# Performance work log

Hardware: AMD Instinct MI355X
Metric: run time of the kernel (lower is better)

The kernel has to match this reference:

```python
import jax, jax.numpy as jnp
import numpy as np
import math

B, S, D = 4, 2048, 1024
H = 1
HD = D // H  # head_dim == hidden_dim since num_heads=1 (required by source's phase_encoder Linear)
HALF = HD // 2
SYNC_LOSS_WEIGHT = 0.01


def setup_inputs() -> dict:
    key = jax.random.key(0)
    ks = jax.random.split(key, 11)
    wstd = 0.02
    inp = {
        "x": jax.random.normal(ks[0], (B, S, D), dtype=jnp.float32),
        "Wq": jax.random.normal(ks[1], (D, D), dtype=jnp.float32) * wstd,
        "bq": jnp.zeros((D,), jnp.float32),
        "Wk": jax.random.normal(ks[2], (D, D), dtype=jnp.float32) * wstd,
        "bk": jnp.zeros((D,), jnp.float32),
        "Wv": jax.random.normal(ks[3], (D, D), dtype=jnp.float32) * wstd,
        "bv": jnp.zeros((D,), jnp.float32),
        "Wp": jax.random.normal(ks[4], (D, D), dtype=jnp.float32) * wstd,
        "bp": jnp.zeros((D,), jnp.float32),
        "Wo": jax.random.normal(ks[5], (D, D), dtype=jnp.float32) * wstd,
        "bo": jnp.zeros((D,), jnp.float32),
        "bifurcation_param": jnp.asarray(1.0, jnp.float32),
        "phase_coupling": jnp.asarray(0.5, jnp.float32),
    }
    return inp


def _phase(t, Wp, bp):
    # t: [B,H,S,HD] -> instantaneous phase via angle(complex(first_half, second_half))
    pf = t @ Wp.T + bp
    re, im = pf[..., :HALF], pf[..., HALF:]
    return jnp.arctan2(im, re)  # [B,H,S,HALF]


def reference(x, Wq, bq, Wk, bk, Wv, bv, Wp, bp, Wo, bo, bifurcation_param, phase_coupling):
    b, s, d = x.shape
    Q = (x @ Wq.T + bq).reshape(b, s, H, HD).transpose(0, 2, 1, 3)  # [B,H,S,HD]
    K = (x @ Wk.T + bk).reshape(b, s, H, HD).transpose(0, 2, 1, 3)
    V = (x @ Wv.T + bv).reshape(b, s, H, HD).transpose(0, 2, 1, 3)

    scores = jnp.einsum("bhqd,bhkd->bhqk", Q, K) / math.sqrt(HD)

    pQ = _phase(Q, Wp, bp)
    pK = _phase(K, Wp, bp)
    # mean_d cos(pQ - pK) == (cos(pQ)@cos(pK)^T + sin(pQ)@sin(pK)^T) / HALF
    sync = (jnp.einsum("bhqd,bhkd->bhqk", jnp.cos(pQ), jnp.cos(pK))
            + jnp.einsum("bhqd,bhkd->bhqk", jnp.sin(pQ), jnp.sin(pK))) / HALF

    t = jnp.tanh(scores)
    bif = bifurcation_param * t * (1.0 - t)

    chaotic = scores + phase_coupling * sync + bif
    attn = jax.nn.softmax(chaotic, axis=-1)

    av = jnp.einsum("bhqk,bhkd->bhqd", attn, V)
    av = av.transpose(0, 2, 1, 3).reshape(b, s, d)
    out = av @ Wo.T + bo

    # torch.var default: unbiased (ddof=1), over last dim of sync
    sync_loss = SYNC_LOSS_WEIGHT * jnp.var(sync, axis=-1, ddof=1).mean()
    return out, sync_loss
```

## Files before the change

kernel.cpp:

```cpp
#include <hip/hip_runtime.h>
#include <hip/hip_bf16.h>
#include <math.h>

#define S_LEN 2048
#define D_MODEL 1024
#define N_BATCH 4
#define N_HALF 512

typedef unsigned short u16;
typedef __attribute__((ext_vector_type(8))) short bf16x8;
typedef __attribute__((ext_vector_type(4))) float f32x4;

__device__ inline u16 f2bf(float v) {
  __hip_bfloat16 h = __float2bfloat16(v);
  return *reinterpret_cast<u16*>(&h);
}
__device__ inline float bf2f(u16 u) {
  __hip_bfloat16 h = *reinterpret_cast<__hip_bfloat16*>(&u);
  return __bfloat162float(h);
}
__device__ inline void gl2lds16(const void* g, void* l) {
  __builtin_amdgcn_global_load_lds(
      (const __attribute__((address_space(1))) unsigned int*)g,
      (__attribute__((address_space(3))) unsigned int*)l, 16, 0, 0);
}
__device__ inline float fast_tanh(float x) {
  float e = __expf(2.0f * x);
  return 1.0f - 2.0f / (e + 1.0f);
}
__device__ inline int xcd_swz(int hw, int n) {
  return (hw & 7) * (n >> 3) + (hw >> 3);
}


#define N0_X   (2097152LL)
#define NW_W   (262144LL)
__global__ __launch_bounds__(256)
void cast_bf4_multi(const float* __restrict__ sx, u16* __restrict__ dx,
                    const float* __restrict__ s1, u16* __restrict__ d1,
                    const float* __restrict__ s2, u16* __restrict__ d2,
                    const float* __restrict__ s3, u16* __restrict__ d3,
                    const float* __restrict__ s4, u16* __restrict__ d4h,
                    u16* __restrict__ d4l) {
  long long i = (long long)blockIdx.x * 256 + threadIdx.x;
  if (i < N0_X) {
    float4 v = ((const float4*)sx)[i];
    ushort4 o;
    o.x = f2bf(v.x); o.y = f2bf(v.y); o.z = f2bf(v.z); o.w = f2bf(v.w);
    ((ushort4*)dx)[i] = o;
    return;
  }
  long long k = i - N0_X;
  int w = (int)(k >> 18);
  long long off = k & (NW_W - 1);
  if (w < 3) {
    const float* s = (w == 0) ? s1 : (w == 1) ? s2 : s3;
    u16* d        = (w == 0) ? d1 : (w == 1) ? d2 : d3;
    float4 v = ((const float4*)s)[off];
    ushort4 o;
    o.x = f2bf(v.x); o.y = f2bf(v.y); o.z = f2bf(v.z); o.w = f2bf(v.w);
    ((ushort4*)d)[off] = o;
  } else {
    float4 v = ((const float4*)s4)[off];
    ushort4 oh, ol;
    float f;
    oh.x = f2bf(v.x); f = v.x - bf2f(oh.x); ol.x = f2bf(f);
    oh.y = f2bf(v.y); f = v.y - bf2f(oh.y); ol.y = f2bf(f);
    oh.z = f2bf(v.z); f = v.z - bf2f(oh.z); ol.z = f2bf(f);
    oh.w = f2bf(v.w); f = v.w - bf2f(oh.w); ol.w = f2bf(f);
    ((ushort4*)d4h)[off] = oh;
    ((ushort4*)d4l)[off] = ol;
  }
}
__global__ __launch_bounds__(256)
void cast_split(const float* __restrict__ src, u16* __restrict__ hi,
                u16* __restrict__ lo, long long n4) {
  long long i = (long long)blockIdx.x * 256 + threadIdx.x;
  if (i >= n4) return;
  float4 v = ((const float4*)src)[i];
  ushort4 oh, ol;
  float f;
  oh.x = f2bf(v.x); f = v.x - bf2f(oh.x); ol.x = f2bf(f);
  oh.y = f2bf(v.y); f = v.y - bf2f(oh.y); ol.y = f2bf(f);
  oh.z = f2bf(v.z); f = v.z - bf2f(oh.z); ol.z = f2bf(f);
  oh.w = f2bf(v.w); f = v.w - bf2f(oh.w); ol.w = f2bf(f);
  ((ushort4*)hi)[i] = oh;
  ((ushort4*)lo)[i] = ol;
}
__global__ __launch_bounds__(256)
void transpose_split(const float* __restrict__ src, u16* __restrict__ hi,
                     u16* __restrict__ lo) {
  __shared__ float t[32][33];
  const int bx = blockIdx.x * 32;
  const int by = blockIdx.y * 32;
  const int c = threadIdx.x & 31;
  const int r0 = (threadIdx.x >> 5) * 4;
#pragma unroll
  for (int r = 0; r < 4; r++)
    t[r0 + r][c] = src[(long long)(by + r0 + r) * D_MODEL + bx + c];
  __syncthreads();
#pragma unroll
  for (int r = 0; r < 4; r++) {
    float v = t[c][r0 + r];
    long long idx = (long long)(bx + r0 + r) * D_MODEL + by + c;
    u16 h = f2bf(v);
    hi[idx] = h;
    lo[idx] = f2bf(v - bf2f(h));
  }
}
__global__ __launch_bounds__(256)
void w2_bias(const float* __restrict__ Wo, const float* __restrict__ bv,
             float* __restrict__ w2b) {
  const int d = blockIdx.x;
  const int tid = threadIdx.x;
  float acc = 0.f;
  for (int j = tid; j < D_MODEL; j += 256)
    acc += Wo[(long long)d * D_MODEL + j] * bv[j];
#pragma unroll
  for (int m = 1; m < 64; m <<= 1) acc += __shfl_xor(acc, m);
  __shared__ float red[4];
  if ((tid & 63) == 0) red[tid >> 6] = acc;
  __syncthreads();
  if (tid == 0) w2b[d] = red[0] + red[1] + red[2] + red[3];
}

__global__ __launch_bounds__(256, 2)
void qk_out3(const u16* __restrict__ X, const u16* __restrict__ Wq,
             const u16* __restrict__ Wk,
             const float* __restrict__ bq, const float* __restrict__ bk,
             u16* __restrict__ Qo, u16* __restrict__ Ko,
             const u16* __restrict__ Ah3, const u16* __restrict__ Al3,
             const u16* __restrict__ Bh3, const u16* __restrict__ Bl3,
             float* __restrict__ W2f) {
  __shared__ __align__(16) u16 smem[4 * 128 * 64];
  const int id   = blockIdx.x;
  const int tid  = threadIdx.x;
  const int wave = tid >> 6;
  const int lane = tid & 63;
  const int quad = lane >> 4;
  const int tc   = lane & 15;
  const int wm = (wave & 1) * 64;
  const int wn = (wave >> 1) * 64;
  const int srow8 = lane >> 3;
  const int scol  = ((lane & 7) ^ srow8) * 8;
  const int srowb = wave * 32;
  const int wb = srowb * 64;
  const long long r8 = 8LL * D_MODEL;
  const int swzA = tc & 7;

  if (id < 64) {
    u16* Ash = smem;
    u16* Asl = smem + 8192;
    u16* Bsh = smem + 16384;
    u16* Bsl = smem + 24576;
    const int bm = (id >> 3) * 128;
    const int bn = (id & 7) * 128;

    f32x4 acc[4][4];
#pragma unroll
    for (int i = 0; i < 4; i++)
#pragma unroll
      for (int j = 0; j < 4; j++) acc[i][j] = (f32x4){0.f, 0.f, 0.f, 0.f};

    long long aoff = (long long)(bm + srowb + srow8) * D_MODEL + scol;
    long long boff = (long long)(bn + srowb + srow8) * D_MODEL + scol;
    const u16 *gah = Ah3 + aoff, *gal = Al3 + aoff;
    const u16 *gbh = Bh3 + boff, *gbl = Bl3 + boff;

    for (int k0 = 0; k0 < D_MODEL; k0 += 64) {
#pragma unroll
      for (int c = 0; c < 4; c++) {
        gl2lds16(gah + c * r8, Ash + wb + c * 512);
        gl2lds16(gal + c * r8, Asl + wb + c * 512);
        gl2lds16(gbh + c * r8, Bsh + wb + c * 512);
        gl2lds16(gbl + c * r8, Bsl + wb + c * 512);
      }
      gah += 64; gal += 64; gbh += 64; gbl += 64;
      __syncthreads();
      bf16x8 ah[4][2], al[4][2], bh[4][2], bl[4][2];
#pragma unroll
      for (int i = 0; i < 4; i++) {
        const int ra = (wm + i * 16 + tc) * 64;
        const int rb = (wn + i * 16 + tc) * 64;
#pragma unroll
        for (int ks = 0; ks < 2; ks++) {
          const int co = ((ks * 4 + quad) ^ swzA) * 8;
          ah[i][ks] = *(const bf16x8*)(Ash + ra + co);
          al[i][ks] = *(const bf16x8*)(Asl + ra + co);
          bh[i][ks] = *(const bf16x8*)(Bsh + rb + co);
          bl[i][ks] = *(const bf16x8*)(Bsl + rb + co);
        }
      }
#pragma unroll
      for (int i = 0; i < 4; i++)
#pragma unroll
        for (int j = 0; j < 4; j++) {
#pragma unroll
          for (int ks = 0; ks < 2; ks++) {
            acc[i][j] = __builtin_amdgcn_mfma_f32_16x16x32_bf16(ah[i][ks], bh[j][ks], acc[i][j], 0, 0, 0);
            acc[i][j] = __builtin_amdgcn_mfma_f32_16x16x32_bf16(ah[i][ks], bl[j][ks], acc[i][j], 0, 0, 0);
            acc[i][j] = __builtin_amdgcn_mfma_f32_16x16x32_bf16(al[i][ks], bh[j][ks], acc[i][j], 0, 0, 0);
          }
        }
      __syncthreads();
    }
#pragma unroll
    for (int i = 0; i < 4; i++) {
      const int row0 = bm + wm + i * 16 + quad * 4;
#pragma unroll
      for (int j = 0; j < 4; j++) {
        const int col = bn + wn + j * 16 + tc;
#pragma unroll
        for (int r = 0; r < 4; r++)
          W2f[(long long)(row0 + r) * D_MODEL + col] = acc[i][j][r];
      }
    }
  } else {
    u16* Xs = smem;
    u16* Qs = smem + 8192;
    u16* Ks = smem + 16384;
    const int qid = xcd_swz(id - 64, 512);
    const int bn = (qid & 7) * 128;
    const int bm = (qid >> 3) * 128;

    f32x4 acc1[4][4], acc2[4][4];
#pragma unroll
    for (int i = 0; i < 4; i++)
#pragma unroll
      for (int j = 0; j < 4; j++) {
        acc1[i][j] = (f32x4){0.f, 0.f, 0.f, 0.f};
        acc2[i][j] = (f32x4){0.f, 0.f, 0.f, 0.f};
      }

    const u16* gx = X  + (long long)(bm + srowb + srow8) * D_MODEL + scol;
    const u16* gq = Wq + (long long)(bn + srowb + srow8) * D_MODEL + scol;
    const u16* gk = Wk + (long long)(bn + srowb + srow8) * D_MODEL + scol;

    for (int k0 = 0; k0 < D_MODEL; k0 += 64) {
#pragma unroll
      for (int c = 0; c < 4; c++) {
        gl2lds16(gx + c * r8, Xs + wb + c * 512);
        gl2lds16(gq + c * r8, Qs + wb + c * 512);
        gl2lds16(gk + c * r8, Ks + wb + c * 512);
      }
      gx += 64; gq += 64; gk += 64;
      __syncthreads();
      bf16x8 af[4][2], bq4[4][2], bk4[4][2];
#pragma unroll
      for (int i = 0; i < 4; i++) {
        const int ra = (wm + i * 16 + tc) * 64;
        const int rb = (wn + i * 16 + tc) * 64;
#pragma unroll
        for (int ks = 0; ks < 2; ks++) {
          const int co = ((ks * 4 + quad) ^ swzA) * 8;
          af[i][ks]  = *(const bf16x8*)(Xs + ra + co);
          bq4[i][ks] = *(const bf16x8*)(Qs + rb + co);
          bk4[i][ks] = *(const bf16x8*)(Ks + rb + co);
        }
      }
#pragma unroll
      for (int i = 0; i < 4; i++)
#pragma unroll
        for (int j = 0; j < 4; j++) {
          acc1[i][j] = __builtin_amdgcn_mfma_f32_16x16x32_bf16(af[i][0], bq4[j][0], acc1[i][j], 0, 0, 0);
          acc2[i][j] = __builtin_amdgcn_mfma_f32_16x16x32_bf16(af[i][0], bk4[j][0], acc2[i][j], 0, 0, 0);
          acc1[i][j] = __builtin_amdgcn_mfma_f32_16x16x32_bf16(af[i][1], bq4[j][1], acc1[i][j], 0, 0, 0);
          acc2[i][j] = __builtin_amdgcn_mfma_f32_16x16x32_bf16(af[i][1], bk4[j][1], acc2[i][j], 0, 0, 0);
        }
      __syncthreads();
    }

#pragma unroll
    for (int i = 0; i < 4; i++) {
      const int row0 = bm + wm + i * 16 + quad * 4;
#pragma unroll
      for (int j = 0; j < 4; j++) {
        const int col = bn + wn + j * 16 + tc;
#pragma unroll
        for (int r = 0; r < 4; r++) {
          long long idx = (long long)(row0 + r) * D_MODEL + col;
          Qo[idx] = f2bf(acc1[i][j][r] + bq[col]);
          Ko[idx] = f2bf(acc2[i][j][r] + bk[col]);
        }
      }
    }
  }
}

__global__ __launch_bounds__(256, 2)
void pf_fused(const u16* __restrict__ Qb, const u16* __restrict__ Wp,
              const float* __restrict__ bp,
              u16* __restrict__ pfQ, u16* __restrict__ pfK,
              long long TDo) {
  __shared__ u16 lds_all[3 * 128 * 64];
  u16* Qs = lds_all;
  u16* Ks = lds_all + 128 * 64;
  u16* Ws = lds_all + 2 * 128 * 64;
  const int tid  = threadIdx.x;
  const int wave = tid >> 6;
  const int lane = tid & 63;
  const int quad = lane >> 4;
  const int tc   = lane & 15;
  const int oid = xcd_swz(blockIdx.x, 512);
  const int bm = (oid >> 3) * 128;
  const int bn = (oid & 7) * 64;
  const int wm = (wave & 1) * 64;
  const int grp = wave >> 1;

  f32x4 acc1[4][4], acc2[4][4];
#pragma unroll
  for (int i = 0; i < 4; i++)
#pragma unroll
    for (int j = 0; j < 4; j++) {
      acc1[i][j] = (f32x4){0.f, 0.f, 0.f, 0.f};
      acc2[i][j] = (f32x4){0.f, 0.f, 0.f, 0.f};
    }

  const int srow8 = lane >> 3;
  const int scol  = ((lane & 7) ^ srow8) * 8;
  const int srowb = wave * 32;
  const u16* gq = Qb + (long long)(bm + srowb + srow8) * D_MODEL + scol;
  const u16* gk = gq + TDo;
  const u16* gw = Wp + (long long)(bn + srowb + srow8 + ((wave & 2) ? 448 : 0)) * D_MODEL + scol;
  const int wb = srowb * 64;
  const long long r8 = 8LL * D_MODEL;
  const int swzA = tc & 7;

  for (int k0 = 0; k0 < D_MODEL; k0 += 64) {
#pragma unroll
    for (int c = 0; c < 4; c++) {
      gl2lds16(gq + c * r8, Qs + wb + c * 512);
      gl2lds16(gk + c * r8, Ks + wb + c * 512);
      gl2lds16(gw + c * r8, Ws + wb + c * 512);
    }
    gq += 64; gk += 64; gw += 64;
    __syncthreads();
    bf16x8 aq[4][2], ak[4][2], bw[4][2];
    const int wn = grp * 64;
#pragma unroll
    for (int i = 0; i < 4; i++) {
      const int ra = (wm + i * 16 + tc) * 64;
      const int rb = (wn + i * 16 + tc) * 64;
#pragma unroll
      for (int ks = 0; ks < 2; ks++) {
        const int co = ((ks * 4 + quad) ^ swzA) * 8;
        aq[i][ks] = *(const bf16x8*)(Qs + ra + co);
        ak[i][ks] = *(const bf16x8*)(Ks + ra + co);
        bw[i][ks] = *(const bf16x8*)(Ws + rb + co);
      }
    }
#pragma unroll
    for (int i = 0; i < 4; i++)
#pragma unroll
      for (int j = 0; j < 4; j++) {
        acc1[i][j] = __builtin_amdgcn_mfma_f32_16x16x32_bf16(aq[i][0], bw[j][0], acc1[i][j], 0, 0, 0);
        acc2[i][j] = __builtin_amdgcn_mfma_f32_16x16x32_bf16(ak[i][0], bw[j][0], acc2[i][j], 0, 0, 0);
        acc1[i][j] = __builtin_amdgcn_mfma_f32_16x16x32_bf16(aq[i][1], bw[j][1], acc1[i][j], 0, 0, 0);
        acc2[i][j] = __builtin_amdgcn_mfma_f32_16x16x32_bf16(ak[i][1], bw[j][1], acc2[i][j], 0, 0, 0);
      }
    __syncthreads();
  }

  float* ex = (float*)lds_all;
  const long long colbase = (long long)bn + (long long)grp * 512;
#pragma unroll
  for (int o = 0; o < 2; o++) {
    u16* Ou = o ? pfK : pfQ;
#pragma unroll
    for (int half = 0; half < 2; half++) {
      int cnt = 0;
#pragma unroll
      for (int i = 2 * half; i < 2 * half + 2; i++)
#pragma unroll
        for (int j = 0; j < 4; j++) {
          f32x4 v = o ? acc2[i][j] : acc1[i][j];
          float b = bp[colbase + j * 16 + tc];
          v[0] += b; v[1] += b; v[2] += b; v[3] += b;
          *(f32x4*)(ex + wave * 2048 + cnt * 256 + lane * 4) = v;
          cnt++;
        }
      __syncthreads();
      cnt = 0;
#pragma unroll
      for (int i = 2 * half; i < 2 * half + 2; i++)
#pragma unroll
        for (int j = 0; j < 4; j++) {
          f32x4 own = *(const f32x4*)(ex + wave * 2048 + cnt * 256 + lane * 4);
          f32x4 oth = *(const f32x4*)(ex + (wave ^ 2) * 2048 + cnt * 256 + lane * 4);
          const int row0 = bm + wm + i * 16 + quad * 4;
          const long long col = colbase + j * 16 + tc;
#pragma unroll
          for (int r = 0; r < 4; r++) {
            float a = own[r], p = oth[r];
            float n2 = a * a + p * p;
            float outv = (grp == 0) ? 1.f : 0.f;
            if (n2 > 0.f) outv = a * (1.0f / sqrtf(n2));
            Ou[(long long)(row0 + r) * D_MODEL + col] = f2bf(outv);
          }
          cnt++;
        }
      __syncthreads();
    }
  }
}

__global__ __launch_bounds__(256, 2)
void chaotic_vwt(const u16* __restrict__ Q, const u16* __restrict__ Kt,
                 const u16* __restrict__ Uq, const u16* __restrict__ Uk,
                 float* __restrict__ Cc,
                 float* __restrict__ ssum, float* __restrict__ ssq,
                 const float* __restrict__ bifp, const float* __restrict__ pcp,
                 const u16* __restrict__ W2h, const u16* __restrict__ W2l,
                 const u16* __restrict__ X, const float* __restrict__ w2b,
                 u16* __restrict__ Ch, u16* __restrict__ Cl,
                 long long sB, long long sC,
                 int interleave, int nchao) {
  __shared__ __align__(16) u16 smem[4 * 128 * 64];
  const int id = xcd_swz(blockIdx.x, (int)gridDim.x);
  int cid = -1, vid = -1;
  if (interleave) {
    if ((id % 3) == 2) vid = id / 3;
    else cid = (id / 3) * 2 + (id % 3);
  } else {
    if (id < nchao) cid = id; else vid = id - nchao;
  }

  const int tid  = threadIdx.x;
  const int wave = tid >> 6;
  const int lane = tid & 63;
  const int quad = lane >> 4;
  const int tc   = lane & 15;
  const int wm = (wave & 1) * 64;
  const int wn = (wave >> 1) * 64;
  const int srow8 = lane >> 3;
  const int scol  = ((lane & 7) ^ srow8) * 8;
  const int srowb = wave * 32;
  const int wb = srowb * 64;
  const long long r8 = 8LL * D_MODEL;
  const int swzA = tc & 7;

  if (cid >= 0) {
    u16* Qs = smem;
    u16* Ks = smem + 8192;
    u16* Us = smem + 16384;
    u16* Ws = smem + 24576;
    const int bn = (cid & 15) * 128;
    const int bm = ((cid >> 4) & 15) * 128;
    const long long z = cid >> 8;
    const long long sQ = (long long)S_LEN * D_MODEL;

    f32x4 acc1[4][4], acc2[4][4];
#pragma unroll
    for (int i = 0; i < 4; i++)
#pragma unroll
      for (int j = 0; j < 4; j++) {
        acc1[i][j] = (f32x4){0.f, 0.f, 0.f, 0.f};
        acc2[i][j] = (f32x4){0.f, 0.f, 0.f, 0.f};
      }

    const u16* gq = Q  + z * sQ + (long long)(bm + srowb + srow8) * D_MODEL + scol;
    const u16* gk = Kt + z * sQ + (long long)(bn + srowb + srow8) * D_MODEL + scol;
    const u16* gu = Uq + z * sQ + (long long)(bm + srowb + srow8) * D_MODEL + scol;
    const u16* gw = Uk + z * sQ + (long long)(bn + srowb + srow8) * D_MODEL + scol;

    for (int k0 = 0; k0 < D_MODEL; k0 += 64) {
#pragma unroll
      for (int c = 0; c < 4; c++) {
        gl2lds16(gq + c * r8, Qs + wb + c * 512);
        gl2lds16(gk + c * r8, Ks + wb + c * 512);
        gl2lds16(gu + c * r8, Us + wb + c * 512);
        gl2lds16(gw + c * r8, Ws + wb + c * 512);
      }
      gq += 64; gk += 64; gu += 64; gw += 64;
      __syncthreads();
      {
        bf16x8 af[4][2], bg[4][2];
#pragma unroll
        for (int i = 0; i < 4; i++) {
          const int ra = (wm + i * 16 + tc) * 64;
          const int rb = (wn + i * 16 + tc) * 64;
#pragma unroll
          for (int ks = 0; ks < 2; ks++) {
            const int co = ((ks * 4 + quad) ^ swzA) * 8;
            af[i][ks] = *(const bf16x8*)(Qs + ra + co);
            bg[i][ks] = *(const bf16x8*)(Ks + rb + co);
          }
        }
#pragma unroll
        for (int i = 0; i < 4; i++)
#pragma unroll
          for (int j = 0; j < 4; j++) {
            acc1[i][j] = __builtin_amdgcn_mfma_f32_16x16x32_bf16(af[i][0], bg[j][0], acc1[i][j], 0, 0, 0);
            acc1[i][j] = __builtin_amdgcn_mfma_f32_16x16x32_bf16(af[i][1], bg[j][1], acc1[i][j], 0, 0, 0);
          }
      }
      {
        bf16x8 cf[4][2], dg[4][2];
#pragma unroll
        for (int i = 0; i < 4; i++) {
          const int ra = (wm + i * 16 + tc) * 64;
          const int rb = (wn + i * 16 + tc) * 64;
#pragma unroll
          for (int ks = 0; ks < 2; ks++) {
            const int co = ((ks * 4 + quad) ^ swzA) * 8;
            cf[i][ks] = *(const bf16x8*)(Us + ra + co);
            dg[i][ks] = *(const bf16x8*)(Ws + rb + co);
          }
        }
#pragma unroll
        for (int i = 0; i < 4; i++)
#pragma unroll
          for (int j = 0; j < 4; j++) {
            acc2[i][j] = __builtin_amdgcn_mfma_f32_16x16x32_bf16(cf[i][0], dg[j][0], acc2[i][j], 0, 0, 0);
            acc2[i][j] = __builtin_amdgcn_mfma_f32_16x16x32_bf16(cf[i][1], dg[j][1], acc2[i][j], 0, 0, 0);
          }
      }
      __syncthreads();
    }

    const float bif = *bifp;
    const float pc  = *pcp;
    float rsum[4][4], rsq[4][4];
#pragma unroll
    for (int i = 0; i < 4; i++)
#pragma unroll
      for (int r = 0; r < 4; r++) { rsum[i][r] = 0.f; rsq[i][r] = 0.f; }

    float* C = Cc + z * (long long)S_LEN * S_LEN;
#pragma unroll
    for (int i = 0; i < 4; i++) {
      const int row0 = bm + wm + i * 16 + quad * 4;
#pragma unroll
      for (int j = 0; j < 4; j++) {
        const int col = bn + wn + j * 16 + tc;
#pragma unroll
        for (int r = 0; r < 4; r++) {
          float sc = acc1[i][j][r] * 0.03125f;
          float sy = acc2[i][j][r] * (1.0f / 512.0f);
          float t  = fast_tanh(sc);
          C[(long long)(row0 + r) * S_LEN + col] = sc + pc * sy + bif * t * (1.0f - t);
          rsum[i][r] += sy;
          rsq[i][r]  += sy * sy;
        }
      }
    }
#pragma unroll
    for (int m = 1; m < 16; m <<= 1) {
#pragma unroll
      for (int i = 0; i < 4; i++)
#pragma unroll
        for (int r = 0; r < 4; r++) {
          rsum[i][r] += __shfl_xor(rsum[i][r], m);
          rsq[i][r]  += __shfl_xor(rsq[i][r], m);
        }
    }
    if (tc == 0) {
#pragma unroll
      for (int i = 0; i < 4; i++)
#pragma unroll
        for (int r = 0; r < 4; r++) {
          long long rr = z * S_LEN + bm + wm + i * 16 + quad * 4 + r;
          atomicAdd(&ssum[rr], rsum[i][r]);
          atomicAdd(&ssq[rr],  rsq[i][r]);
        }
    }
  } else {
    u16* Ah = smem;
    u16* Al = smem + 8192;
    u16* Bs = smem + 16384;
    const int bn = (vid & 15) * 128;
    const int bm = ((vid >> 4) & 7) * 128;
    const long long z = vid >> 7;

    f32x4 acc[4][4];
#pragma unroll
    for (int i = 0; i < 4; i++)
#pragma unroll
      for (int j = 0; j < 4; j++) acc[i][j] = (f32x4){0.f, 0.f, 0.f, 0.f};

    const long long aoff = (long long)(bm + srowb + srow8) * D_MODEL + scol;
    const u16* gah = W2h + aoff;
    const u16* gal = W2l + aoff;
    const u16* gb  = X + z * sB + (long long)(bn + srowb + srow8) * D_MODEL + scol;

    for (int k0 = 0; k0 < D_MODEL; k0 += 64) {
#pragma unroll
      for (int c = 0; c < 4; c++) {
        gl2lds16(gah + c * r8, Ah + wb + c * 512);
        gl2lds16(gal + c * r8, Al + wb + c * 512);
        gl2lds16(gb  + c * r8, Bs + wb + c * 512);
      }
      gah += 64; gal += 64; gb += 64;
      __syncthreads();
      bf16x8 ah4[4][2], al4[4][2], bx[4][2];
#pragma unroll
      for (int i = 0; i < 4; i++) {
        const int ra = (wm + i * 16 + tc) * 64;
        const int rb = (wn + i * 16 + tc) * 64;
#pragma unroll
        for (int ks = 0; ks < 2; ks++) {
          const int co = ((ks * 4 + quad) ^ swzA) * 8;
          ah4[i][ks] = *(const bf16x8*)(Ah + ra + co);
          al4[i][ks] = *(const bf16x8*)(Al + ra + co);
          bx[i][ks]  = *(const bf16x8*)(Bs + rb + co);
        }
      }
#pragma unroll
      for (int i = 0; i < 4; i++)
#pragma unroll
        for (int j = 0; j < 4; j++) {
          acc[i][j] = __builtin_amdgcn_mfma_f32_16x16x32_bf16(ah4[i][0], bx[j][0], acc[i][j], 0, 0, 0);
          acc[i][j] = __builtin_amdgcn_mfma_f32_16x16x32_bf16(al4[i][0], bx[j][0], acc[i][j], 0, 0, 0);
          acc[i][j] = __builtin_amdgcn_mfma_f32_16x16x32_bf16(ah4[i][1], bx[j][1], acc[i][j], 0, 0, 0);
          acc[i][j] = __builtin_amdgcn_mfma_f32_16x16x32_bf16(al4[i][1], bx[j][1], acc[i][j], 0, 0, 0);
        }
      __syncthreads();
    }

    u16* Chz = Ch + z * sC;
    u16* Clz = Cl + z * sC;
#pragma unroll
    for (int i = 0; i < 4; i++) {
      const int row0 = bm + wm + i * 16 + quad * 4;
#pragma unroll
      for (int j = 0; j < 4; j++) {
        const int col = bn + wn + j * 16 + tc;
#pragma unroll
        for (int r = 0; r < 4; r++) {
          float v = acc[i][j][r] + w2b[row0 + r];
          long long idx = (long long)(row0 + r) * S_LEN + col;
          u16 h = f2bf(v);
          Chz[idx] = h;
          Clz[idx] = f2bf(v - bf2f(h));
        }
      }
    }
  }
}

__global__ __launch_bounds__(256)
void gemm_bsplit(const u16* __restrict__ A,
                 const u16* __restrict__ Bh, const u16* __restrict__ Bl,
                 const float* __restrict__ bias, float* __restrict__ C,
                 int N, int K, long long sA, long long sB, long long sC) {
  __shared__ u16 As[128 * 64];
  __shared__ u16 Bsh[128 * 64];
  __shared__ u16 Bsl[128 * 64];
  const int tid  = threadIdx.x;
  const int wave = tid >> 6;
  const int lane = tid & 63;
  const int quad = lane >> 4;
  const int tc   = lane & 15;
  const int oid = xcd_swz(blockIdx.x, (int)gridDim.x);
  const int bn = (oid & 7) * 128;
  const int bm = ((oid >> 3) & 15) * 128;
  const long long z = oid >> 7;
  const int wm = (wave & 1) * 64;
  const int wn = (wave >> 1) * 64;

  f32x4 acc[4][4];
#pragma unroll
  for (int i = 0; i < 4; i++)
#pragma unroll
    for (int j = 0; j < 4; j++) acc[i][j] = (f32x4){0.f, 0.f, 0.f, 0.f};

  const int srow8 = lane >> 3;
  const int scol  = ((lane & 7) ^ srow8) * 8;
  const int srowb = wave * 32;
  const long long boff = (long long)(bn + srowb + srow8) * K + scol;
  const u16* ga  = A + z * sA + (long long)(bm + srowb + srow8) * K + scol;
  const u16* gbh = Bh + z * sB + boff;
  const u16* gbl = Bl + z * sB + boff;
  const int wb = srowb * 64;
  const long long r8K = 8LL * K;
  const int swzA = tc & 7;

  for (int k0 = 0; k0 < K; k0 += 64) {
#pragma unroll
    for (int c = 0; c < 4; c++) {
      gl2lds16(ga  + c * r8K, As  + wb + c * 512);
      gl2lds16(gbh + c * r8K, Bsh + wb + c * 512);
      gl2lds16(gbl + c * r8K, Bsl + wb + c * 512);
    }
    ga += 64; gbh += 64; gbl += 64;
    __syncthreads();
    bf16x8 af[4][2], bh[4][2], bl[4][2];
#pragma unroll
    for (int i = 0; i < 4; i++) {
      const int ra = (wm + i * 16 + tc) * 64;
      const int rb = (wn + i * 16 + tc) * 64;
#pragma unroll
      for (int ks = 0; ks < 2; ks++) {
        const int co = ((ks * 4 + quad) ^ swzA) * 8;
        af[i][ks] = *(const bf16x8*)(As  + ra + co);
        bh[i][ks] = *(const bf16x8*)(Bsh + rb + co);
        bl[i][ks] = *(const bf16x8*)(Bsl + rb + co);
      }
    }
#pragma unroll
    for (int i = 0; i < 4; i++)
#pragma unroll
      for (int j = 0; j < 4; j++) {
        acc[i][j] = __builtin_amdgcn_mfma_f32_16x16x32_bf16(af[i][0], bh[j][0], acc[i][j], 0, 0, 0);
        acc[i][j] = __builtin_amdgcn_mfma_f32_16x16x32_bf16(af[i][0], bl[j][0], acc[i][j], 0, 0, 0);
        acc[i][j] = __builtin_amdgcn_mfma_f32_16x16x32_bf16(af[i][1], bh[j][1], acc[i][j], 0, 0, 0);
        acc[i][j] = __builtin_amdgcn_mfma_f32_16x16x32_bf16(af[i][1], bl[j][1], acc[i][j], 0, 0, 0);
      }
    __syncthreads();
  }

  float* Cz = C + z * sC;
#pragma unroll
  for (int i = 0; i < 4; i++) {
    const int row0 = bm + wm + i * 16 + quad * 4;
#pragma unroll
    for (int j = 0; j < 4; j++) {
      const int col = bn + wn + j * 16 + tc;
#pragma unroll
      for (int r = 0; r < 4; r++)
        Cz[(long long)(row0 + r) * N + col] = acc[i][j][r] + bias[col];
    }
  }
}

__global__ __launch_bounds__(256)
void softmax_bf(const float* __restrict__ Cc, u16* __restrict__ P) {
  const long long row = (long long)blockIdx.y * S_LEN + blockIdx.x;
  const int tid = threadIdx.x;
  const float* p = Cc + row * S_LEN + tid * 8;
  u16* q = P + row * S_LEN + tid * 8;
  float4 a = *(const float4*)p;
  float4 b = *(const float4*)(p + 4);
  float v[8] = {a.x, a.y, a.z, a.w, b.x, b.y, b.z, b.w};
  float m = v[0];
#pragma unroll
  for (int i = 1; i < 8; i++) m = fmaxf(m, v[i]);
#pragma unroll
  for (int mask = 1; mask < 64; mask <<= 1) m = fmaxf(m, __shfl_xor(m, mask));
  __shared__ float red[8];
  if ((tid & 63) == 0) red[tid >> 6] = m;
  __syncthreads();
  m = fmaxf(fmaxf(red[0], red[1]), fmaxf(red[2], red[3]));
  float s = 0.f;
#pragma unroll
  for (int i = 0; i < 8; i++) { v[i] = __expf(v[i] - m); s += v[i]; }
#pragma unroll
  for (int mask = 1; mask < 64; mask <<= 1) s += __shfl_xor(s, mask);
  __syncthreads();
  if ((tid & 63) == 0) red[4 + (tid >> 6)] = s;
  __syncthreads();
  s = red[4] + red[5] + red[6] + red[7];
  float inv = 1.0f / s;
  ushort4 o0, o1;
  o0.x = f2bf(v[0] * inv); o0.y = f2bf(v[1] * inv);
  o0.z = f2bf(v[2] * inv); o0.w = f2bf(v[3] * inv);
  o1.x = f2bf(v[4] * inv); o1.y = f2bf(v[5] * inv);
  o1.z = f2bf(v[6] * inv); o1.w = f2bf(v[7] * inv);
  *(ushort4*)q = o0;
  *(ushort4*)(q + 4) = o1;
}

__global__ __launch_bounds__(1024)
void syncloss_kernel(const float* __restrict__ ssum, const float* __restrict__ ssq,
                     float* __restrict__ out) {
  const int tid = threadIdx.x;
  float acc = 0.f;
  for (int r = tid; r < N_BATCH * S_LEN; r += 1024) {
    float su = ssum[r], sq = ssq[r];
    acc += (sq - su * su * (1.0f / 2048.0f)) * (1.0f / 2047.0f);
  }
#pragma unroll
  for (int mask = 1; mask < 64; mask <<= 1) acc += __shfl_xor(acc, mask);
  __shared__ float red[16];
  if ((tid & 63) == 0) red[tid >> 6] = acc;
  __syncthreads();
  if (tid == 0) {
    float t = 0.f;
#pragma unroll
    for (int k = 0; k < 16; k++) t += red[k];
    out[0] = 0.01f * (t / (float)(N_BATCH * S_LEN));
  }
}

extern "C" void kernel_launch(void* const* d_in, const int* in_sizes, int n_in,
                              void* d_out, int out_size, void* d_ws, size_t ws_size,
                              hipStream_t stream) {
  const float* x    = (const float*)d_in[0];
  const float* Wq   = (const float*)d_in[1];
  const float* bq   = (const float*)d_in[2];
  const float* Wk   = (const float*)d_in[3];
  const float* bk   = (const float*)d_in[4];
  const float* Wv   = (const float*)d_in[5];
  const float* bv   = (const float*)d_in[6];
  const float* Wp   = (const float*)d_in[7];
  const float* bp   = (const float*)d_in[8];
  const float* Wo   = (const float*)d_in[9];
  const float* bo   = (const float*)d_in[10];
  const float* bifp = (const float*)d_in[11];
  const float* pcp  = (const float*)d_in[12];
  float* out = (float*)d_out;

  const long long NROW = (long long)N_BATCH * S_LEN;
  const long long TD   = NROW * D_MODEL;
  const long long WSZ  = (long long)D_MODEL * D_MODEL;

  u16* xbf   = (u16*)d_ws;
  u16* wqb   = xbf + TD;
  u16* wkb   = wqb + WSZ;
  u16* wpb   = wkb + WSZ;
  u16* woh   = wpb + WSZ;
  u16* wol   = woh + WSZ;
  u16* wvth  = wol + WSZ;
  u16* wvtl  = wvth + WSZ;
  u16* w2h   = wvtl + WSZ;
  u16* w2l   = w2h + WSZ;
  float* W2f = (float*)(w2l + WSZ);
  float* w2b = W2f + WSZ;
  u16* Qbf   = (u16*)(w2b + D_MODEL);
  u16* Kbf   = Qbf + TD;
  u16* pfQ   = Kbf + TD;
  u16* pfK   = pfQ + TD;
  float* Cc  = (float*)(pfK + TD);
  float* ssum = Cc + (long long)N_BATCH * S_LEN * S_LEN;
  float* ssq  = ssum + NROW;
  u16* attn = Qbf;
  u16* vwh  = pfQ;
  u16* vwl  = pfK;
  u16* vwh2 = (u16*)(ssq + NROW);
  u16* vwl2 = vwh2 + TD;
  const size_t need = (size_t)((char*)(vwl2 + TD) - (char*)d_ws);
  const bool fused = (ws_size >= need);

  dim3 blk(256);
  const long long sQ = (long long)S_LEN * D_MODEL;
  const long long sS = (long long)S_LEN * S_LEN;

  cast_bf4_multi<<<12288, blk, 0, stream>>>(x, xbf, Wq, wqb, Wk, wkb, Wp, wpb,
                                            Wo, woh, wol);
  transpose_split<<<dim3(32, 32), blk, 0, stream>>>(Wv, wvth, wvtl);
  qk_out3<<<576, blk, 0, stream>>>(xbf, wqb, wkb, bq, bk, Qbf, Kbf,
                                   woh, wol, wvth, wvtl, W2f);
  cast_split<<<(int)(WSZ / 4 / 256), blk, 0, stream>>>(W2f, w2h, w2l, WSZ / 4);
  w2_bias<<<D_MODEL, blk, 0, stream>>>(Wo, bv, w2b);

  pf_fused<<<512, blk, 0, stream>>>(Qbf, wpb, bp, pfQ, pfK, TD);
  hipMemsetAsync(ssum, 0, (size_t)(2 * NROW) * sizeof(float), stream);

  if (fused) {
    chaotic_vwt<<<1536, blk, 0, stream>>>(
        Qbf, Kbf, pfQ, pfK, Cc, ssum, ssq, bifp, pcp,
        w2h, w2l, xbf, w2b, vwh2, vwl2, sQ, sQ, 1, 1024);
  } else {
    chaotic_vwt<<<1024, blk, 0, stream>>>(
        Qbf, Kbf, pfQ, pfK, Cc, ssum, ssq, bifp, pcp,
        w2h, w2l, xbf, w2b, vwh, vwl, sQ, sQ, 0, 1024);
    chaotic_vwt<<<512, blk, 0, stream>>>(
        Qbf, Kbf, pfQ, pfK, Cc, ssum, ssq, bifp, pcp,
        w2h, w2l, xbf, w2b, vwh, vwl, sQ, sQ, 0, 0);
  }

  softmax_bf<<<dim3(S_LEN, N_BATCH), blk, 0, stream>>>(Cc, attn);
  gemm_bsplit<<<512, blk, 0, stream>>>(
      attn, fused ? vwh2 : vwh, fused ? vwl2 : vwl, bo, out,
      D_MODEL, S_LEN, sS, sQ, sQ);
  syncloss_kernel<<<1, 1024, 0, stream>>>(ssum, ssq, out + TD);
}
```

Measured before the change: 444.8 us.

## Merge prep kernels, fuse hi/lo split into GEMM epilogue, remap tiles for L2 locality

Folds the cast, Wv transpose-split and Wo·bv bias kernels into one prep launch, and writes the W2 product directly as bf16 hi/lo from the qk_out3 epilogue, which removes the cast_split kernel and the fp32 W2f round trip. It also remaps block-to-tile indices in several GEMMs into grouped 4x4 or 2x4 supertiles within each chunk to improve L2 reuse of A and B tiles. The cost is more branching in a single large prep kernel, and the transpose path there now shares a block with a shared-memory barrier.

```diff
diff --git a/kernel.cpp b/kernel.cpp
--- a/kernel.cpp
+++ b/kernel.cpp
@@ -36,92 +36,84 @@
 #define N0_X   (2097152LL)
 #define NW_W   (262144LL)
 __global__ __launch_bounds__(256)
-void cast_bf4_multi(const float* __restrict__ sx, u16* __restrict__ dx,
-                    const float* __restrict__ s1, u16* __restrict__ d1,
-                    const float* __restrict__ s2, u16* __restrict__ d2,
-                    const float* __restrict__ s3, u16* __restrict__ d3,
-                    const float* __restrict__ s4, u16* __restrict__ d4h,
-                    u16* __restrict__ d4l) {
-  long long i = (long long)blockIdx.x * 256 + threadIdx.x;
-  if (i < N0_X) {
-    float4 v = ((const float4*)sx)[i];
-    ushort4 o;
-    o.x = f2bf(v.x); o.y = f2bf(v.y); o.z = f2bf(v.z); o.w = f2bf(v.w);
-    ((ushort4*)dx)[i] = o;
+void prep_multi(const float* __restrict__ sx, u16* __restrict__ dx,
+                const float* __restrict__ s1, u16* __restrict__ d1,
+                const float* __restrict__ s2, u16* __restrict__ d2,
+                const float* __restrict__ s3, u16* __restrict__ d3,
+                const float* __restrict__ s4, u16* __restrict__ d4h,
+                u16* __restrict__ d4l,
+                const float* __restrict__ Wv, u16* __restrict__ wvth,
+                u16* __restrict__ wvtl,
+                const float* __restrict__ Wo, const float* __restrict__ bv,
+                float* __restrict__ w2b) {
+  __shared__ float tsh[32][33];
+  const int bid = blockIdx.x;
+  const int tid = threadIdx.x;
+  if (bid < 12288) {
+    long long i = (long long)bid * 256 + tid;
+    if (i < N0_X) {
+      float4 v = ((const float4*)sx)[i];
+      ushort4 o;
+      o.x = f2bf(v.x); o.y = f2bf(v.y); o.z = f2bf(v.z); o.w = f2bf(v.w);
+      ((ushort4*)dx)[i] = o;
+      return;
+    }
+    long long k = i - N0_X;
+    int w = (int)(k >> 18);
+    long long off = k & (NW_W - 1);
+    if (w < 3) {
+      const float* s = (w == 0) ? s1 : (w == 1) ? s2 : s3;
+      u16* d        = (w == 0) ? d1 : (w == 1) ? d2 : d3;
+      float4 v = ((const float4*)s)[off];
+      ushort4 o;
+      o.x = f2bf(v.x); o.y = f2bf(v.y); o.z = f2bf(v.z); o.w = f2bf(v.w);
+      ((ushort4*)d)[off] = o;
+    } else {
+      float4 v = ((const float4*)s4)[off];
+      ushort4 oh, ol;
+      float f;
+      oh.x = f2bf(v.x); f = v.x - bf2f(oh.x); ol.x = f2bf(f);
+      oh.y = f2bf(v.y); f = v.y - bf2f(oh.y); ol.y = f2bf(f);
+      oh.z = f2bf(v.z); f = v.z - bf2f(oh.z); ol.z = f2bf(f);
+      oh.w = f2bf(v.w); f = v.w - bf2f(oh.w); ol.w = f2bf(f);
+      ((ushort4*)d4h)[off] = oh;
+      ((ushort4*)d4l)[off] = ol;
+    }
     return;
   }
-  long long k = i - N0_X;
-  int w = (int)(k >> 18);
-  long long off = k & (NW_W - 1);
-  if (w < 3) {
-    const float* s = (w == 0) ? s1 : (w == 1) ? s2 : s3;
-    u16* d        = (w == 0) ? d1 : (w == 1) ? d2 : d3;
-    float4 v = ((const float4*)s)[off];
-    ushort4 o;
-    o.x = f2bf(v.x); o.y = f2bf(v.y); o.z = f2bf(v.z); o.w = f2bf(v.w);
-    ((ushort4*)d)[off] = o;
-  } else {
-    float4 v = ((const float4*)s4)[off];
-    ushort4 oh, ol;
-    float f;
-    oh.x = f2bf(v.x); f = v.x - bf2f(oh.x); ol.x = f2bf(f);
-    oh.y = f2bf(v.y); f = v.y - bf2f(oh.y); ol.y = f2bf(f);
-    oh.z = f2bf(v.z); f = v.z - bf2f(oh.z); ol.z = f2bf(f);
-    oh.w = f2bf(v.w); f = v.w - bf2f(oh.w); ol.w = f2bf(f);
-    ((ushort4*)d4h)[off] = oh;
-    ((ushort4*)d4l)[off] = ol;
-  }
-}
-__global__ __launch_bounds__(256)
-void cast_split(const float* __restrict__ src, u16* __restrict__ hi,
-                u16* __restrict__ lo, long long n4) {
-  long long i = (long long)blockIdx.x * 256 + threadIdx.x;
-  if (i >= n4) return;
-  float4 v = ((const float4*)src)[i];
-  ushort4 oh, ol;
-  float f;
-  oh.x = f2bf(v.x); f = v.x - bf2f(oh.x); ol.x = f2bf(f);
-  oh.y = f2bf(v.y); f = v.y - bf2f(oh.y); ol.y = f2bf(f);
-  oh.z = f2bf(v.z); f = v.z - bf2f(oh.z); ol.z = f2bf(f);
-  oh.w = f2bf(v.w); f = v.w - bf2f(oh.w); ol.w = f2bf(f);
-  ((ushort4*)hi)[i] = oh;
-  ((ushort4*)lo)[i] = ol;
-}
-__global__ __launch_bounds__(256)
-void transpose_split(const float* __restrict__ src, u16* __restrict__ hi,
-                     u16* __restrict__ lo) {
-  __shared__ float t[32][33];
-  const int bx = blockIdx.x * 32;
-  const int by = blockIdx.y * 32;
-  const int c = threadIdx.x & 31;
-  const int r0 = (threadIdx.x >> 5) * 4;
-#pragma unroll
-  for (int r = 0; r < 4; r++)
-    t[r0 + r][c] = src[(long long)(by + r0 + r) * D_MODEL + bx + c];
-  __syncthreads();
-#pragma unroll
-  for (int r = 0; r < 4; r++) {
-    float v = t[c][r0 + r];
-    long long idx = (long long)(bx + r0 + r) * D_MODEL + by + c;
-    u16 h = f2bf(v);
-    hi[idx] = h;
-    lo[idx] = f2bf(v - bf2f(h));
-  }
-}
-__global__ __launch_bounds__(256)
-void w2_bias(const float* __restrict__ Wo, const float* __restrict__ bv,
-             float* __restrict__ w2b) {
-  const int d = blockIdx.x;
-  const int tid = threadIdx.x;
-  float acc = 0.f;
-  for (int j = tid; j < D_MODEL; j += 256)
-    acc += Wo[(long long)d * D_MODEL + j] * bv[j];
-#pragma unroll
-  for (int m = 1; m < 64; m <<= 1) acc += __shfl_xor(acc, m);
-  __shared__ float red[4];
-  if ((tid & 63) == 0) red[tid >> 6] = acc;
-  __syncthreads();
-  if (tid == 0) w2b[d] = red[0] + red[1] + red[2] + red[3];
+  if (bid < 13312) {
+    const int b2 = bid - 12288;
+    const int bx = (b2 & 31) * 32;
+    const int by = (b2 >> 5) * 32;
+    const int c = tid & 31;
+    const int r0 = (tid >> 5) * 4;
+#pragma unroll
+    for (int r = 0; r < 4; r++)
+      tsh[r0 + r][c] = Wv[(long long)(by + r0 + r) * D_MODEL + bx + c];
+    __syncthreads();
+#pragma unroll
+    for (int r = 0; r < 4; r++) {
+      float v = tsh[c][r0 + r];
+      long long idx = (long long)(bx + r0 + r) * D_MODEL + by + c;
+      u16 h = f2bf(v);
+      wvth[idx] = h;
+      wvtl[idx] = f2bf(v - bf2f(h));
+    }
+    return;
+  }
+  const int base = (bid - 13312) * 16;
+  const int wave = tid >> 6;
+  const int lane = tid & 63;
+#pragma unroll
+  for (int rr = 0; rr < 4; rr++) {
+    const int d = base + wave * 4 + rr;
+    float acc = 0.f;
+    for (int j = lane; j < D_MODEL; j += 64)
+      acc += Wo[(long long)d * D_MODEL + j] * bv[j];
+#pragma unroll
+    for (int m = 1; m < 64; m <<= 1) acc += __shfl_xor(acc, m);
+    if (lane == 0) w2b[d] = acc;
+  }
 }
 
 __global__ __launch_bounds__(256, 2)
@@ -131,7 +123,7 @@
              u16* __restrict__ Qo, u16* __restrict__ Ko,
              const u16* __restrict__ Ah3, const u16* __restrict__ Al3,
              const u16* __restrict__ Bh3, const u16* __restrict__ Bl3,
-             float* __restrict__ W2f) {
+             u16* __restrict__ w2h, u16* __restrict__ w2l) {
   __shared__ __align__(16) u16 smem[4 * 128 * 64];
   const int id   = blockIdx.x;
   const int tid  = threadIdx.x;
@@ -211,17 +203,25 @@
       for (int j = 0; j < 4; j++) {
         const int col = bn + wn + j * 16 + tc;
 #pragma unroll
-        for (int r = 0; r < 4; r++)
-          W2f[(long long)(row0 + r) * D_MODEL + col] = acc[i][j][r];
+        for (int r = 0; r < 4; r++) {
+          long long idx = (long long)(row0 + r) * D_MODEL + col;
+          float v = acc[i][j][r];
+          u16 h = f2bf(v);
+          w2h[idx] = h;
+          w2l[idx] = f2bf(v - bf2f(h));
+        }
       }
     }
   } else {
     u16* Xs = smem;
     u16* Qs = smem + 8192;
     u16* Ks = smem + 16384;
-    const int qid = xcd_swz(id - 64, 512);
-    const int bn = (qid & 7) * 128;
-    const int bm = (qid >> 3) * 128;
+    const int qs = xcd_swz(id - 64, 512);
+    const int chunk = qs >> 6;
+    const int t = qs & 63;
+    const int st = t >> 4, sp = t & 15;
+    const int bn = (((st & 1) << 2) + (sp & 3)) * 128;
+    const int bm = (chunk * 8 + ((st >> 1) << 2) + (sp >> 2)) * 128;
 
     f32x4 acc1[4][4], acc2[4][4];
 #pragma unroll
@@ -302,8 +302,11 @@
   const int quad = lane >> 4;
   const int tc   = lane & 15;
   const int oid = xcd_swz(blockIdx.x, 512);
-  const int bm = (oid >> 3) * 128;
-  const int bn = (oid & 7) * 64;
+  const int chunk = oid >> 6;
+  const int t = oid & 63;
+  const int st = t >> 4, sp = t & 15;
+  const int bn = (((st & 1) << 2) + (sp & 3)) * 64;
+  const int bm = (chunk * 8 + ((st >> 1) << 2) + (sp >> 2)) * 128;
   const int wm = (wave & 1) * 64;
   const int grp = wave >> 1;
 
@@ -444,9 +447,12 @@
     u16* Ks = smem + 8192;
     u16* Us = smem + 16384;
     u16* Ws = smem + 24576;
-    const int bn = (cid & 15) * 128;
-    const int bm = ((cid >> 4) & 15) * 128;
-    const long long z = cid >> 8;
+    const int chunk = cid >> 7;
+    const int t = cid & 127;
+    const int st = t >> 4, sp = t & 15;
+    const int bn = (((st & 3) << 2) + (sp & 3)) * 128;
+    const int bm = (((chunk & 1) << 3) + ((st >> 2) << 2) + (sp >> 2)) * 128;
+    const long long z = chunk >> 1;
     const long long sQ = (long long)S_LEN * D_MODEL;
 
     f32x4 acc1[4][4], acc2[4][4];
@@ -537,8 +543,8 @@
         for (int r = 0; r < 4; r++) {
           float sc = acc1[i][j][r] * 0.03125f;
           float sy = acc2[i][j][r] * (1.0f / 512.0f);
-          float t  = fast_tanh(sc);
-          C[(long long)(row0 + r) * S_LEN + col] = sc + pc * sy + bif * t * (1.0f - t);
+          float t2 = fast_tanh(sc);
+          C[(long long)(row0 + r) * S_LEN + col] = sc + pc * sy + bif * t2 * (1.0f - t2);
           rsum[i][r] += sy;
           rsq[i][r]  += sy * sy;
         }
@@ -568,9 +574,11 @@
     u16* Ah = smem;
     u16* Al = smem + 8192;
     u16* Bs = smem + 16384;
-    const int bn = (vid & 15) * 128;
-    const int bm = ((vid >> 4) & 7) * 128;
-    const long long z = vid >> 7;
+    const int chunk = vid >> 6;
+    const int t = vid & 63;
+    const int bn = (((t >> 4) << 2) + (t & 3)) * 128;
+    const int bm = (((chunk & 1) << 2) + ((t >> 2) & 3)) * 128;
+    const long long z = chunk >> 1;
 
     f32x4 acc[4][4];
 #pragma unroll
@@ -652,9 +660,12 @@
   const int quad = lane >> 4;
   const int tc   = lane & 15;
   const int oid = xcd_swz(blockIdx.x, (int)gridDim.x);
-  const int bn = (oid & 7) * 128;
-  const int bm = ((oid >> 3) & 15) * 128;
-  const long long z = oid >> 7;
+  const int chunk = oid >> 6;
+  const int t = oid & 63;
+  const int st = t >> 3, sp = t & 7;
+  const int bn = ((((st & 3) << 1) + (sp & 1))) * 128;
+  const int bm = ((((chunk & 1) << 3) + ((st >> 2) << 2) + (sp >> 1))) * 128;
+  const long long z = chunk >> 1;
   const int wm = (wave & 1) * 64;
   const int wn = (wave >> 1) * 64;
 
@@ -835,13 +846,11 @@
   const long long sQ = (long long)S_LEN * D_MODEL;
   const long long sS = (long long)S_LEN * S_LEN;
 
-  cast_bf4_multi<<<12288, blk, 0, stream>>>(x, xbf, Wq, wqb, Wk, wkb, Wp, wpb,
-                                            Wo, woh, wol);
-  transpose_split<<<dim3(32, 32), blk, 0, stream>>>(Wv, wvth, wvtl);
+  prep_multi<<<13376, blk, 0, stream>>>(x, xbf, Wq, wqb, Wk, wkb, Wp, wpb,
+                                        Wo, woh, wol, Wv, wvth, wvtl,
+                                        Wo, bv, w2b);
   qk_out3<<<576, blk, 0, stream>>>(xbf, wqb, wkb, bq, bk, Qbf, Kbf,
-                                   woh, wol, wvth, wvtl, W2f);
-  cast_split<<<(int)(WSZ / 4 / 256), blk, 0, stream>>>(W2f, w2h, w2l, WSZ / 4);
-  w2_bias<<<D_MODEL, blk, 0, stream>>>(Wo, bv, w2b);
+                                   woh, wol, wvth, wvtl, w2h, w2l);
 
   pf_fused<<<512, blk, 0, stream>>>(Qbf, wpb, bp, pfQ, pfK, TD);
   hipMemsetAsync(ssum, 0, (size_t)(2 * NROW) * sizeof(float), stream);
```

Result: slower. 464.8 us (+4.5%).

## Fuse W2 hi/lo split into GEMM epilogue and remap tile order for L2 locality

Applied to the files above, without the earlier changes.

The W2 = Wo·Wv GEMM epilogue now writes the bf16 hi/lo split directly instead of writing fp32 and running a separate cast_split kernel. This removes one launch and an fp32 round trip through memory. The block-to-tile mapping in chaotic_vwt is also remapped so that groups of 16 blocks cover 4x4 neighbourhoods of tiles, which is meant to raise L2 reuse of the Q/K and W2/X operands. The epilogue stores become scattered 2-byte writes, which may be less coalesced.

```diff
diff --git a/kernel.cpp b/kernel.cpp
--- a/kernel.cpp
+++ b/kernel.cpp
@@ -73,21 +73,6 @@
   }
 }
 __global__ __launch_bounds__(256)
-void cast_split(const float* __restrict__ src, u16* __restrict__ hi,
-                u16* __restrict__ lo, long long n4) {
-  long long i = (long long)blockIdx.x * 256 + threadIdx.x;
-  if (i >= n4) return;
-  float4 v = ((const float4*)src)[i];
-  ushort4 oh, ol;
-  float f;
-  oh.x = f2bf(v.x); f = v.x - bf2f(oh.x); ol.x = f2bf(f);
-  oh.y = f2bf(v.y); f = v.y - bf2f(oh.y); ol.y = f2bf(f);
-  oh.z = f2bf(v.z); f = v.z - bf2f(oh.z); ol.z = f2bf(f);
-  oh.w = f2bf(v.w); f = v.w - bf2f(oh.w); ol.w = f2bf(f);
-  ((ushort4*)hi)[i] = oh;
-  ((ushort4*)lo)[i] = ol;
-}
-__global__ __launch_bounds__(256)
 void transpose_split(const float* __restrict__ src, u16* __restrict__ hi,
                      u16* __restrict__ lo) {
   __shared__ float t[32][33];
@@ -131,7 +116,7 @@
              u16* __restrict__ Qo, u16* __restrict__ Ko,
              const u16* __restrict__ Ah3, const u16* __restrict__ Al3,
              const u16* __restrict__ Bh3, const u16* __restrict__ Bl3,
-             float* __restrict__ W2f) {
+             u16* __restrict__ w2h, u16* __restrict__ w2l) {
   __shared__ __align__(16) u16 smem[4 * 128 * 64];
   const int id   = blockIdx.x;
   const int tid  = threadIdx.x;
@@ -211,8 +196,13 @@
       for (int j = 0; j < 4; j++) {
         const int col = bn + wn + j * 16 + tc;
 #pragma unroll
-        for (int r = 0; r < 4; r++)
-          W2f[(long long)(row0 + r) * D_MODEL + col] = acc[i][j][r];
+        for (int r = 0; r < 4; r++) {
+          long long idx = (long long)(row0 + r) * D_MODEL + col;
+          float v = acc[i][j][r];
+          u16 h = f2bf(v);
+          w2h[idx] = h;
+          w2l[idx] = f2bf(v - bf2f(h));
+        }
       }
     }
   } else {
@@ -444,9 +434,12 @@
     u16* Ks = smem + 8192;
     u16* Us = smem + 16384;
     u16* Ws = smem + 24576;
-    const int bn = (cid & 15) * 128;
-    const int bm = ((cid >> 4) & 15) * 128;
-    const long long z = cid >> 8;
+    const int chunk = cid >> 7;
+    const int t = cid & 127;
+    const int st = t >> 4, sp = t & 15;
+    const int bn = (((st & 3) << 2) + (sp & 3)) * 128;
+    const int bm = (((chunk & 1) << 3) + ((st >> 2) << 2) + (sp >> 2)) * 128;
+    const long long z = chunk >> 1;
     const long long sQ = (long long)S_LEN * D_MODEL;
 
     f32x4 acc1[4][4], acc2[4][4];
@@ -537,8 +530,8 @@
         for (int r = 0; r < 4; r++) {
           float sc = acc1[i][j][r] * 0.03125f;
           float sy = acc2[i][j][r] * (1.0f / 512.0f);
-          float t  = fast_tanh(sc);
-          C[(long long)(row0 + r) * S_LEN + col] = sc + pc * sy + bif * t * (1.0f - t);
+          float t2 = fast_tanh(sc);
+          C[(long long)(row0 + r) * S_LEN + col] = sc + pc * sy + bif * t2 * (1.0f - t2);
           rsum[i][r] += sy;
           rsq[i][r]  += sy * sy;
         }
@@ -568,9 +561,11 @@
     u16* Ah = smem;
     u16* Al = smem + 8192;
     u16* Bs = smem + 16384;
-    const int bn = (vid & 15) * 128;
-    const int bm = ((vid >> 4) & 7) * 128;
-    const long long z = vid >> 7;
+    const int chunk = vid >> 6;
+    const int t = vid & 63;
+    const int bn = (((t >> 4) << 2) + (t & 3)) * 128;
+    const int bm = (((chunk & 1) << 2) + ((t >> 2) & 3)) * 128;
+    const long long z = chunk >> 1;
 
     f32x4 acc[4][4];
 #pragma unroll
@@ -839,8 +834,7 @@
                                             Wo, woh, wol);
   transpose_split<<<dim3(32, 32), blk, 0, stream>>>(Wv, wvth, wvtl);
   qk_out3<<<576, blk, 0, stream>>>(xbf, wqb, wkb, bq, bk, Qbf, Kbf,
-                                   woh, wol, wvth, wvtl, W2f);
-  cast_split<<<(int)(WSZ / 4 / 256), blk, 0, stream>>>(W2f, w2h, w2l, WSZ / 4);
+                                   woh, wol, wvth, wvtl, w2h, w2l);
   w2_bias<<<D_MODEL, blk, 0, stream>>>(Wo, bv, w2b);
 
   pf_fused<<<512, blk, 0, stream>>>(Qbf, wpb, bp, pfQ, pfK, TD);
```

After: 437.6 us. No clear change (-1.6%).
